# Kernel optimization log

Hardware: AMD Instinct MI355X
Metric: run time of the kernel (lower is better)

## Reference

```python
import jax, jax.numpy as jnp
import numpy as np

B, T, H, NC = 64, 512, 1000, 2000
WV, PV, IV, TV, MV = 100000, 50, 5, 20, 500
FEAT = 300 + 4 * 50  # 500
EPS = 1e-5


def setup_inputs() -> dict:
    key = jax.random.key(0)
    ks = jax.random.split(key, 32)

    def emb(k, v, d):
        t = jax.random.normal(k, (v, d), jnp.float32) * 0.1
        return t.at[0].set(0.0)  # padding_idx=0

    def unif(k, shape, s):
        return jax.random.uniform(k, shape, jnp.float32, -s, s)

    s = 1.0 / np.sqrt(H)
    inp = {}
    inp['word_idxs'] = jax.random.randint(ks[0], (B, T), 0, WV)
    inp['pos_idxs'] = jax.random.randint(ks[1], (B, T), 0, PV)
    inp['iob_idxs'] = jax.random.randint(ks[2], (B, T), 0, IV)
    inp['type_idxs'] = jax.random.randint(ks[3], (B, T), 0, TV)
    inp['mention_idxs'] = jax.random.randint(ks[4], (B, T), 0, MV)
    lengths = jnp.sort(jax.random.randint(ks[5], (B,), 1, T + 1))[::-1]
    inp['lengths'] = lengths.at[0].set(T)  # descending, max == T
    inp['hidden'] = jnp.zeros((2, B, H), jnp.float32)
    inp['word_emb'] = emb(ks[6], WV, 300)
    inp['pos_emb'] = emb(ks[7], PV, 50)
    inp['iob_emb'] = emb(ks[8], IV, 50)
    inp['type_emb'] = emb(ks[9], TV, 50)
    inp['mention_emb'] = emb(ks[10], MV, 50)
    inp['w_ih_fwd'] = unif(ks[11], (3 * H, FEAT), s)
    inp['w_hh_fwd'] = unif(ks[12], (3 * H, H), s)
    inp['b_ih_fwd'] = unif(ks[13], (3 * H,), s)
    inp['b_hh_fwd'] = unif(ks[14], (3 * H,), s)
    inp['w_ih_bwd'] = unif(ks[15], (3 * H, FEAT), s)
    inp['w_hh_bwd'] = unif(ks[16], (3 * H, H), s)
    inp['b_ih_bwd'] = unif(ks[17], (3 * H,), s)
    inp['b_hh_bwd'] = unif(ks[18], (3 * H,), s)
    inp['lin_w'] = unif(ks[19], (NC, 2 * H), 1.0 / np.sqrt(2 * H))
    inp['lin_b'] = unif(ks[20], (NC,), 1.0 / np.sqrt(2 * H))
    inp['bn_gamma'] = 1.0 + 0.1 * jax.random.normal(ks[21], (NC,), jnp.float32)
    inp['bn_beta'] = 0.1 * jax.random.normal(ks[22], (NC,), jnp.float32)
    inp['bn_mean'] = 0.1 * jax.random.normal(ks[23], (NC,), jnp.float32)
    inp['bn_var'] = jax.random.uniform(ks[24], (NC,), jnp.float32, 0.5, 1.5)
    return inp


def _gru_dir(x_proj, mask, h0, w_hh, b_hh):
    """x_proj: [T,B,3H] precomputed input projections; mask: [T,B] validity."""
    def step(h, tm):
        xp, m = tm
        hp = h @ w_hh.T + b_hh  # [B,3H]
        xr, xz, xn = jnp.split(xp, 3, axis=-1)
        hr, hz, hn = jnp.split(hp, 3, axis=-1)
        r = jax.nn.sigmoid(xr + hr)
        z = jax.nn.sigmoid(xz + hz)
        n = jnp.tanh(xn + r * hn)
        h_new = (1.0 - z) * n + z * h
        h = jnp.where(m[:, None], h_new, h)  # freeze past sequence end (packed semantics)
        return h, None
    hT, _ = jax.lax.scan(step, h0, (x_proj, mask))
    return hT


def reference(word_idxs, pos_idxs, iob_idxs, type_idxs, mention_idxs, lengths, hidden,
              word_emb, pos_emb, iob_emb, type_emb, mention_emb,
              w_ih_fwd, w_hh_fwd, b_ih_fwd, b_hh_fwd,
              w_ih_bwd, w_hh_bwd, b_ih_bwd, b_hh_bwd,
              lin_w, lin_b, bn_gamma, bn_beta, bn_mean, bn_var):
    # multi-embedding concat -> [B,T,500]; eval mode: dropouts identity
    feat = jnp.concatenate([
        word_emb[word_idxs], pos_emb[pos_idxs], iob_emb[iob_idxs],
        type_emb[type_idxs], mention_emb[mention_idxs]], axis=-1)
    valid = (jnp.arange(T)[None, :] < lengths[:, None])  # [B,T]

    # forward direction
    xpf = jnp.einsum('btf,gf->tbg', feat, w_ih_fwd) + b_ih_fwd  # [T,B,3H]
    h_f = _gru_dir(xpf, valid.T, hidden[0], w_hh_fwd, b_hh_fwd)

    # backward direction: reverse the valid portion of each sequence
    rev_idx = jnp.clip(lengths[:, None] - 1 - jnp.arange(T)[None, :], 0, T - 1)  # [B,T]
    feat_r = jnp.take_along_axis(feat, rev_idx[:, :, None], axis=1)
    xpb = jnp.einsum('btf,gf->tbg', feat_r, w_ih_bwd) + b_ih_bwd
    h_b = _gru_dir(xpb, valid.T, hidden[1], w_hh_bwd, b_hh_bwd)

    h_cat = jnp.concatenate([h_f, h_b], axis=-1)  # [B,2H]
    logits = h_cat @ lin_w.T + lin_b
    out = bn_gamma * (logits - bn_mean) * jax.lax.rsqrt(bn_var + EPS) + bn_beta
    hidden_out = jnp.stack([h_f, h_b])  # [2,B,H] like PyTorch GRU final hidden
    return out, hidden_out
```

## Files before the change

### kernel.cpp

```cpp
#include <hip/hip_runtime.h>
#include <hip/hip_bf16.h>

typedef __attribute__((ext_vector_type(8))) short bf16x8;
typedef __attribute__((ext_vector_type(4))) float f32x4;

#define MFMA16(a,b,c) __builtin_amdgcn_mfma_f32_16x16x32_bf16((a),(b),(c),0,0,0)

__device__ __forceinline__ float sigmf(float x){ return 1.f/(1.f + __expf(-x)); }
__device__ __forceinline__ float tanh_fast(float x){
    float e = __expf(-2.f*fabsf(x));
    float t = (1.f-e)/(1.f+e);
    return x < 0.f ? -t : t;
}

#define AS1 __attribute__((address_space(1)))
#define AS3 __attribute__((address_space(3)))
__device__ __forceinline__ void gll16(const void* g, void* l) {
    __builtin_amdgcn_global_load_lds((const AS1 unsigned int*)g, (AS3 unsigned int*)l, 16, 0, 0);
}

__device__ __forceinline__ bf16x8 load16_asm(const __hip_bfloat16* p) {
    bf16x8 v;
    asm volatile("global_load_dwordx4 %0, %1, off" : "=v"(v) : "v"(p));
    return v;
}
__device__ __forceinline__ bf16x8 load16_sc(const __hip_bfloat16* p) {
    bf16x8 v;
    asm volatile("global_load_dwordx4 %0, %1, off sc0 sc1" : "=v"(v) : "v"(p) : "memory");
    return v;
}
__device__ __forceinline__ void store2_sc(__hip_bfloat16* p, float v) {
    __hip_bfloat16 b = __float2bfloat16(v);
    unsigned int u = *reinterpret_cast<unsigned short*>(&b);
    asm volatile("global_store_short %0, %1, off sc0 sc1" :: "v"(p), "v"(u) : "memory");
}
__device__ __forceinline__ void store4_sc(unsigned* p, unsigned v) {
    asm volatile("global_store_dword %0, %1, off sc0 sc1" :: "v"(p), "v"(v) : "memory");
}
__device__ __forceinline__ unsigned poll_sc(const unsigned* p) {
    unsigned v;
    asm volatile("global_load_dword %0, %1, off sc0 sc1\n\ts_waitcnt vmcnt(0)"
                 : "=v"(v) : "v"(p) : "memory");
    return v;
}
__device__ __forceinline__ unsigned ld2_g(const __hip_bfloat16* p) {
    unsigned v;
    asm volatile("global_load_ushort %0, %1, off" : "=v"(v) : "v"(p));
    return v;
}

#define B_   64
#define T_   512
#define H_   1000
#define HP   1024
#define G3   3072
#define NC_  2000
#define FEAT_C 500
#define FEAT_P 512
#define NROWS 32768

#define OFF_FEAT  ((size_t)0)
#define OFF_WIHF  (OFF_FEAT + 33554432ull)
#define OFF_WIHB  (OFF_WIHF + 3145728ull)
#define OFF_WHH   (OFF_WIHB + 3145728ull)
#define OFF_LINW  (OFF_WHH + 12582912ull)
#define OFF_BIHF  (OFF_LINW + 8192000ull)
#define OFF_BIHB  (OFF_BIHF + 12288ull)
#define OFF_BHH   (OFF_BIHB + 12288ull)
#define OFF_XP    (OFF_BHH + 24576ull)
#define OFF_HBF   (OFF_XP + 402653184ull)
#define OFF_HCAT  (OFF_HBF + 524288ull)
#define OFF_BAR   (OFF_HCAT + 262144ull)
#define WS_NEED   (OFF_BAR + 1024ull)

__global__ void cvt_pad_3h(const float* __restrict__ src, __hip_bfloat16* __restrict__ dst,
                           int C, int Cp) {
    size_t i = (size_t)blockIdx.x*blockDim.x + threadIdx.x;
    size_t total = (size_t)G3 * Cp;
    if (i >= total) return;
    int r = (int)(i / Cp), c = (int)(i % Cp);
    int chunk = r >> 10, j = r & 1023;
    float v = (j < H_ && c < C) ? src[((size_t)chunk*H_ + j)*C + c] : 0.f;
    dst[i] = __float2bfloat16(v);
}

__global__ void cvt_pad(const float* __restrict__ src, __hip_bfloat16* __restrict__ dst,
                        int R, int C, int Cp) {
    size_t i = (size_t)blockIdx.x*blockDim.x + threadIdx.x;
    size_t total = (size_t)R * Cp;
    if (i >= total) return;
    int r = (int)(i / Cp), c = (int)(i % Cp);
    float v = (c < C) ? src[(size_t)r*C + c] : 0.f;
    dst[i] = __float2bfloat16(v);
}

__global__ void pad_b3h(const float* __restrict__ src, float* __restrict__ dst) {
    int i = blockIdx.x*blockDim.x + threadIdx.x;
    if (i >= G3) return;
    int chunk = i >> 10, j = i & 1023;
    dst[i] = (j < H_) ? src[chunk*H_ + j] : 0.f;
}

__global__ __launch_bounds__(256)
void embed_k(const int* __restrict__ wi, const int* __restrict__ pi, const int* __restrict__ ii,
             const int* __restrict__ ti, const int* __restrict__ mi,
             const float* __restrict__ we, const float* __restrict__ pe, const float* __restrict__ ie,
             const float* __restrict__ te, const float* __restrict__ me,
             __hip_bfloat16* __restrict__ feat) {
    int r = blockIdx.x;
    int iw = wi[r], ip = pi[r], ib = ii[r], it = ti[r], im = mi[r];
    #pragma unroll
    for (int q = 0; q < 2; ++q) {
        int c = threadIdx.x + q*256;
        float v;
        if      (c < 300) v = we[(size_t)iw*300 + c];
        else if (c < 350) v = pe[ip*50 + (c-300)];
        else if (c < 400) v = ie[ib*50 + (c-350)];
        else if (c < 450) v = te[it*50 + (c-400)];
        else if (c < 500) v = me[im*50 + (c-450)];
        else              v = 0.f;
        feat[(size_t)r*FEAT_P + c] = __float2bfloat16(v);
    }
}

__global__ __launch_bounds__(256)
void gemm_xp(const __hip_bfloat16* __restrict__ feat,
             const __hip_bfloat16* __restrict__ W,
             const float* __restrict__ bias,
             const int* __restrict__ lengths,
             __hip_bfloat16* __restrict__ xp,
             int dir) {
    __shared__ char smem_raw[32768];
    __hip_bfloat16* As = (__hip_bfloat16*)smem_raw;
    __hip_bfloat16* Bs = (__hip_bfloat16*)(smem_raw + 16384);
    const int tid = threadIdx.x;
    const int wave = tid >> 6, lane = tid & 63;
    const int bm = blockIdx.x, bn = blockIdx.y;
    const int wm = wave >> 1, wn = wave & 1;

    int arow_src[4];
    #pragma unroll
    for (int q = 0; q < 4; ++q) {
        int flat = q*256 + tid;
        int row = flat >> 3;
        int r_g = bm*128 + row;
        int t = r_g >> 6, b = r_g & 63;
        int src_t;
        if (dir == 0) src_t = t;
        else { int L = lengths[b]; src_t = L - 1 - t; src_t = src_t < 0 ? 0 : src_t; }
        arow_src[q] = b*T_ + src_t;
    }

    f32x4 acc[4][4];
    #pragma unroll
    for (int i = 0; i < 4; ++i)
        #pragma unroll
        for (int j = 0; j < 4; ++j) acc[i][j] = (f32x4){0.f,0.f,0.f,0.f};

    for (int kt = 0; kt < 8; ++kt) {
        int k0 = kt*64;
        #pragma unroll
        for (int q = 0; q < 4; ++q) {
            int flat = q*256 + tid;
            int row = flat >> 3, c8 = flat & 7;
            gll16(feat + (size_t)arow_src[q]*FEAT_P + k0 + c8*8,
                  As + (q*256 + wave*64)*8);
            gll16(W + (size_t)(bn*128 + row)*FEAT_P + k0 + c8*8,
                  Bs + (q*256 + wave*64)*8);
        }
        __syncthreads();
        #pragma unroll
        for (int ks = 0; ks < 2; ++ks) {
            bf16x8 af[4], bfr[4];
            #pragma unroll
            for (int i = 0; i < 4; ++i)
                af[i] = *(const bf16x8*)(As + (wm*64 + i*16 + (lane&15))*64 + ks*32 + (lane>>4)*8);
            #pragma unroll
            for (int j = 0; j < 4; ++j)
                bfr[j] = *(const bf16x8*)(Bs + (wn*64 + j*16 + (lane&15))*64 + ks*32 + (lane>>4)*8);
            #pragma unroll
            for (int i = 0; i < 4; ++i)
                #pragma unroll
                for (int j = 0; j < 4; ++j)
                    acc[i][j] = MFMA16(af[i], bfr[j], acc[i][j]);
        }
        __syncthreads();
    }

    __hip_bfloat16* Cs = (__hip_bfloat16*)smem_raw;
    #pragma unroll
    for (int j = 0; j < 4; ++j) {
        int col_l = wn*64 + j*16 + (lane & 15);
        float bs = bias[bn*128 + col_l];
        #pragma unroll
        for (int i = 0; i < 4; ++i) {
            #pragma unroll
            for (int r = 0; r < 4; ++r) {
                int row_l = wm*64 + i*16 + (lane>>4)*4 + r;
                Cs[row_l*128 + col_l] = __float2bfloat16(acc[i][j][r] + bs);
            }
        }
    }
    __syncthreads();
    #pragma unroll
    for (int q = 0; q < 8; ++q) {
        int flat = q*256 + tid;
        int row = flat >> 4, c8 = flat & 15;
        bf16x8 v = *(const bf16x8*)(Cs + row*128 + c8*8);
        *(bf16x8*)(xp + (size_t)(bm*128 + row)*G3 + bn*128 + c8*8) = v;
    }
}

__global__ void init_h(const float* __restrict__ hidden, __hip_bfloat16* __restrict__ hbf) {
    int i = blockIdx.x*blockDim.x + threadIdx.x;
    if (i >= 2*B_*HP) return;
    int row = i >> 10, j = i & 1023;
    int dir = row >> 6, b = row & 63;
    float v = (j < H_) ? hidden[((size_t)dir*B_ + b)*H_ + j] : 0.f;
    __hip_bfloat16 bv = __float2bfloat16(v);
    hbf[i] = bv;
    hbf[2*B_*HP + i] = bv;
}

__global__ void bar_init(unsigned* bar) { if (threadIdx.x < 256) bar[threadIdx.x] = 0u; }

__global__ __attribute__((amdgpu_flat_work_group_size(512,512), amdgpu_waves_per_eu(2,2)))
void gru_persist(const __hip_bfloat16* __restrict__ whh,
                 const float* __restrict__ bhh,
                 const __hip_bfloat16* __restrict__ xp,
                 const int* __restrict__ lengths,
                 const float* __restrict__ hidden,
                 __hip_bfloat16* __restrict__ hbf,
                 __hip_bfloat16* __restrict__ hcat,
                 float* __restrict__ hid_o,
                 unsigned* __restrict__ bar) {
    __shared__ float part[2][4][3][256];
    const int blk = blockIdx.x;
    const int r8  = blk & 7, q8 = blk >> 3;
    const int g   = r8 >> 1;
    const int dir = g >> 1, bh = g & 1;
    const int ug  = q8*2 + (r8 & 1);
    const int w    = threadIdx.x >> 6;
    const int lane = threadIdx.x & 63;
    const int bg  = w >> 2;
    const int kh  = w & 3;
    const int u   = lane & 15;
    const int rg  = lane >> 4;

    const int j   = ug*16 + u;
    const int bA  = bh*32 + bg*16 + u;
    const int bF  = bh*32 + bg*16 + rg*4 + kh;
    const int myLen  = lengths[bF];
    const int lenBlk = lengths[bh*32];

    unsigned* slots = bar + g*64;

    const float bhr = bhh[dir*G3 + j];
    const float bhz = bhh[dir*G3 + HP + j];
    const float bhn = bhh[dir*G3 + 2*HP + j];
    float hreg = (j < H_) ? hidden[((size_t)dir*B_ + bF)*H_ + j] : 0.f;

    bf16x8 wf0[8], wf1[8], wf2[8];
    {
        const __hip_bfloat16* wb = whh + (size_t)dir*G3*HP + (size_t)j*HP + kh*256 + rg*8;
        #pragma unroll
        for (int ks = 0; ks < 8; ++ks) {
            wf0[ks] = load16_asm(wb + ks*32);
            wf1[ks] = load16_asm(wb + (size_t)HP*HP + ks*32);
            wf2[ks] = load16_asm(wb + (size_t)2*HP*HP + ks*32);
        }
        asm volatile("s_waitcnt vmcnt(0)" ::: "memory");
        __builtin_amdgcn_sched_barrier(0);
    }

    const size_t hrowA = (size_t)(dir*B_ + bA)*HP + kh*256 + rg*8;
    const size_t hidxF = (size_t)(dir*B_ + bF)*HP + j;
    const size_t xbase = (size_t)dir*NROWS*G3 + (size_t)bF*G3 + j;

    unsigned pxr, pxz, pxn;
    {
        const __hip_bfloat16* x0 = xp + xbase;
        pxr = ld2_g(x0); pxz = ld2_g(x0 + HP); pxn = ld2_g(x0 + 2*HP);
        asm volatile("s_waitcnt vmcnt(0)" ::: "memory");
    }

    for (int t = 0; t < lenBlk; ++t) {
        const int cur = t & 1, prev = cur ^ 1;
        const __hip_bfloat16* ha = hbf + (size_t)prev*2*B_*HP + hrowA;
        bf16x8 af[8];
        #pragma unroll
        for (int ks = 0; ks < 8; ++ks) af[ks] = load16_sc(ha + ks*32);
        asm volatile("s_waitcnt vmcnt(0)" ::: "memory");
        __builtin_amdgcn_sched_barrier(0);

        f32x4 a0 = {0.f,0.f,0.f,0.f}, a1 = {0.f,0.f,0.f,0.f}, a2 = {0.f,0.f,0.f,0.f};
        #pragma unroll
        for (int ks = 0; ks < 8; ++ks) {
            a0 = MFMA16(af[ks], wf0[ks], a0);
            a1 = MFMA16(af[ks], wf1[ks], a1);
            a2 = MFMA16(af[ks], wf2[ks], a2);
        }

        float xr = __uint_as_float(pxr << 16);
        float xz = __uint_as_float(pxz << 16);
        float xn = __uint_as_float(pxn << 16);

        {
            int tn = (t + 1 < lenBlk) ? t + 1 : t;
            const __hip_bfloat16* xnp = xp + xbase + (size_t)tn*B_*G3;
            pxr = ld2_g(xnp); pxz = ld2_g(xnp + HP); pxn = ld2_g(xnp + 2*HP);
        }

        *(f32x4*)&part[bg][kh][0][lane*4] = a0;
        *(f32x4*)&part[bg][kh][1][lane*4] = a1;
        *(f32x4*)&part[bg][kh][2][lane*4] = a2;
        __syncthreads();
        float sr = 0.f, sz = 0.f, sn = 0.f;
        #pragma unroll
        for (int q = 0; q < 4; ++q) {
            sr += part[bg][q][0][lane*4 + kh];
            sz += part[bg][q][1][lane*4 + kh];
            sn += part[bg][q][2][lane*4 + kh];
        }
        float rr = sigmf(xr + sr + bhr);
        float zz = sigmf(xz + sz + bhz);
        float nn = tanh_fast(xn + rr*(sn + bhn));
        float hnew = (t < myLen) ? ((1.f - zz)*nn + zz*hreg) : hreg;
        hreg = hnew;
        store2_sc(hbf + (size_t)cur*2*B_*HP + hidxF, hnew);
        asm volatile("s_waitcnt vmcnt(0)" ::: "memory");
        __syncthreads();

        if (t + 1 < lenBlk) {
            if (w == 0) {
                if (lane == 0) store4_sc(&slots[ug], (unsigned)(t + 1));
                const unsigned tgt = (unsigned)(t + 1);
                for (;;) {
                    unsigned v = poll_sc(slots + lane);
                    if (__all((int)(v >= tgt))) break;
                    __builtin_amdgcn_s_sleep(1);
                }
            }
            __syncthreads();
        }
    }

    if (j < H_) {
        hid_o[((size_t)dir*B_ + bF)*H_ + j] = hreg;
        hcat[(size_t)bF*2048 + dir*H_ + j] = __float2bfloat16(hreg);
    }
}

__global__ __launch_bounds__(256)
void lin_bn_k(const __hip_bfloat16* __restrict__ hcat,
              const __hip_bfloat16* __restrict__ linw,
              const float* __restrict__ lin_b, const float* __restrict__ gamma,
              const float* __restrict__ beta, const float* __restrict__ mean,
              const float* __restrict__ var,
              float* __restrict__ out) {
    __shared__ __hip_bfloat16 wlds[16*2056];
    const int n0 = blockIdx.x*16;
    const int tid = threadIdx.x;
    #pragma unroll
    for (int q = 0; q < 16; ++q) {
        int flat8 = q*256 + tid;
        int row = flat8 >> 8, c8 = flat8 & 255;
        bf16x8 v = *(const bf16x8*)(linw + (size_t)(n0+row)*2048 + c8*8);
        *(bf16x8*)(wlds + row*2056 + c8*8) = v;
    }
    __syncthreads();
    const int wave = tid >> 6, lane = tid & 63;
    const int mrow = wave*16 + (lane & 15);
    f32x4 acc = {0.f,0.f,0.f,0.f};
    for (int ks = 0; ks < 64; ++ks) {
        bf16x8 a = *(const bf16x8*)(hcat + (size_t)mrow*2048 + ks*32 + (lane>>4)*8);
        bf16x8 b = *(const bf16x8*)(wlds + (lane&15)*2056 + ks*32 + (lane>>4)*8);
        acc = MFMA16(a, b, acc);
    }
    const int c = n0 + (lane & 15);
    const float g = gamma[c], bt = beta[c], mn = mean[c], lb = lin_b[c];
    const float iv = rsqrtf(var[c] + 1e-5f);
    #pragma unroll
    for (int r = 0; r < 4; ++r) {
        int b_ = wave*16 + (lane>>4)*4 + r;
        float logit = acc[r] + lb;
        out[(size_t)b_*NC_ + c] = g*(logit - mn)*iv + bt;
    }
}

extern "C" void kernel_launch(void* const* d_in, const int* in_sizes, int n_in,
                              void* d_out, int out_size, void* d_ws, size_t ws_size,
                              hipStream_t stream) {
    const int*   wi      = (const int*)d_in[0];
    const int*   pi      = (const int*)d_in[1];
    const int*   ii      = (const int*)d_in[2];
    const int*   ti      = (const int*)d_in[3];
    const int*   mi      = (const int*)d_in[4];
    const int*   lengths = (const int*)d_in[5];
    const float* hidden  = (const float*)d_in[6];
    const float* we      = (const float*)d_in[7];
    const float* pe      = (const float*)d_in[8];
    const float* ie      = (const float*)d_in[9];
    const float* te      = (const float*)d_in[10];
    const float* me      = (const float*)d_in[11];
    const float* w_ih_f  = (const float*)d_in[12];
    const float* w_hh_f  = (const float*)d_in[13];
    const float* b_ih_f  = (const float*)d_in[14];
    const float* b_hh_f  = (const float*)d_in[15];
    const float* w_ih_b  = (const float*)d_in[16];
    const float* w_hh_b  = (const float*)d_in[17];
    const float* b_ih_b  = (const float*)d_in[18];
    const float* b_hh_b  = (const float*)d_in[19];
    const float* lin_w   = (const float*)d_in[20];
    const float* lin_b   = (const float*)d_in[21];
    const float* gamma   = (const float*)d_in[22];
    const float* beta    = (const float*)d_in[23];
    const float* mean    = (const float*)d_in[24];
    const float* var     = (const float*)d_in[25];
    float* out = (float*)d_out;

    if (ws_size < WS_NEED) return;

    char* ws = (char*)d_ws;
    __hip_bfloat16* FEAT = (__hip_bfloat16*)(ws + OFF_FEAT);
    __hip_bfloat16* WIHF = (__hip_bfloat16*)(ws + OFF_WIHF);
    __hip_bfloat16* WIHB = (__hip_bfloat16*)(ws + OFF_WIHB);
    __hip_bfloat16* WHH  = (__hip_bfloat16*)(ws + OFF_WHH);
    __hip_bfloat16* LINW = (__hip_bfloat16*)(ws + OFF_LINW);
    float* BIHF = (float*)(ws + OFF_BIHF);
    float* BIHB = (float*)(ws + OFF_BIHB);
    float* BHH  = (float*)(ws + OFF_BHH);
    __hip_bfloat16* XP   = (__hip_bfloat16*)(ws + OFF_XP);
    __hip_bfloat16* HBF  = (__hip_bfloat16*)(ws + OFF_HBF);
    __hip_bfloat16* HCAT = (__hip_bfloat16*)(ws + OFF_HCAT);
    unsigned* BAR = (unsigned*)(ws + OFF_BAR);
    float* HIDO = out + (size_t)B_*NC_;

    cvt_pad_3h<<<(G3*512 + 255)/256, 256, 0, stream>>>(w_ih_f, WIHF, FEAT_C, FEAT_P);
    cvt_pad_3h<<<(G3*512 + 255)/256, 256, 0, stream>>>(w_ih_b, WIHB, FEAT_C, FEAT_P);
    cvt_pad_3h<<<(G3*1024 + 255)/256, 256, 0, stream>>>(w_hh_f, WHH, H_, HP);
    cvt_pad_3h<<<(G3*1024 + 255)/256, 256, 0, stream>>>(w_hh_b, WHH + (size_t)G3*HP, H_, HP);
    cvt_pad<<<(NC_*2048 + 255)/256, 256, 0, stream>>>(lin_w, LINW, NC_, NC_, 2048);
    pad_b3h<<<(G3 + 255)/256, 256, 0, stream>>>(b_ih_f, BIHF);
    pad_b3h<<<(G3 + 255)/256, 256, 0, stream>>>(b_ih_b, BIHB);
    pad_b3h<<<(G3 + 255)/256, 256, 0, stream>>>(b_hh_f, BHH);
    pad_b3h<<<(G3 + 255)/256, 256, 0, stream>>>(b_hh_b, BHH + G3);

    embed_k<<<NROWS, 256, 0, stream>>>(wi, pi, ii, ti, mi, we, pe, ie, te, me, FEAT);

    dim3 gg(NROWS/128, G3/128);
    gemm_xp<<<gg, 256, 0, stream>>>(FEAT, WIHF, BIHF, lengths, XP, 0);
    gemm_xp<<<gg, 256, 0, stream>>>(FEAT, WIHB, BIHB, lengths, XP + (size_t)NROWS*G3, 1);

    init_h<<<(2*B_*HP + 255)/256, 256, 0, stream>>>(hidden, HBF);
    bar_init<<<1, 256, 0, stream>>>(BAR);
    {
        void* args[] = { (void*)&WHH, (void*)&BHH, (void*)&XP, (void*)&lengths,
                         (void*)&hidden, (void*)&HBF, (void*)&HCAT, (void*)&HIDO, (void*)&BAR };
        hipLaunchCooperativeKernel((const void*)gru_persist, dim3(256), dim3(512),
                                   args, 0, stream);
    }

    lin_bn_k<<<NC_/16, 256, 0, stream>>>(HCAT, LINW, lin_b, gamma, beta, mean, var, out);
}
```

Measured before the change: 3.490 ms.

## Repartition persistent GRU across 128 blocks with LDS-staged hidden state

Reworks the persistent GRU kernel from 256 blocks in groups of 64 over 32 batches to 128 blocks in groups of 16 over 16 batches per direction. Each block now loads its 16-row hidden slice into LDS once and shares it across waves, keeps twice as many W_hh fragments in registers per wave, and uses a two-way K split instead of a four-way one. Input projections are fetched as 16-byte vector loads staged through LDS rather than per-thread scalar loads. Barrier slots are spaced onto separate cache lines and each group waits on only 16 peers. In exchange, half as many CUs run the step, there is more register pressure, and there is an extra LDS round-trip and __syncthreads per step.

```diff
diff --git a/kernel.cpp b/kernel.cpp
--- a/kernel.cpp
+++ b/kernel.cpp
@@ -43,11 +43,9 @@
                  : "=v"(v) : "v"(p) : "memory");
     return v;
 }
-__device__ __forceinline__ unsigned ld2_g(const __hip_bfloat16* p) {
-    unsigned v;
-    asm volatile("global_load_ushort %0, %1, off" : "=v"(v) : "v"(p));
-    return v;
-}
+
+#define VDRAIN() do { asm volatile("s_waitcnt vmcnt(0)" ::: "memory"); \
+                      __builtin_amdgcn_sched_barrier(0); } while (0)
 
 #define B_   64
 #define T_   512
@@ -58,6 +56,11 @@
 #define FEAT_C 500
 #define FEAT_P 512
 #define NROWS 32768
+
+#define HROW 2064
+#define OFF_PART  (16*HROW)
+#define OFF_XPLDS (OFF_PART + 12288)
+#define SMEM_SZ   (OFF_XPLDS + 6144)
 
 #define OFF_FEAT  ((size_t)0)
 #define OFF_WIHF  (OFF_FEAT + 33554432ull)
@@ -71,7 +74,7 @@
 #define OFF_HBF   (OFF_XP + 402653184ull)
 #define OFF_HCAT  (OFF_HBF + 524288ull)
 #define OFF_BAR   (OFF_HCAT + 262144ull)
-#define WS_NEED   (OFF_BAR + 1024ull)
+#define WS_NEED   (OFF_BAR + 8192ull)
 
 __global__ void cvt_pad_3h(const float* __restrict__ src, __hip_bfloat16* __restrict__ dst,
                            int C, int Cp) {
@@ -222,7 +225,10 @@
     hbf[2*B_*HP + i] = bv;
 }
 
-__global__ void bar_init(unsigned* bar) { if (threadIdx.x < 256) bar[threadIdx.x] = 0u; }
+__global__ void bar_init(unsigned* bar) {
+    int i = blockIdx.x*blockDim.x + threadIdx.x;
+    if (i < 2048) bar[i] = 0u;
+}
 
 __global__ __attribute__((amdgpu_flat_work_group_size(512,512), amdgpu_waves_per_eu(2,2)))
 void gru_persist(const __hip_bfloat16* __restrict__ whh,
@@ -234,109 +240,137 @@
                  __hip_bfloat16* __restrict__ hcat,
                  float* __restrict__ hid_o,
                  unsigned* __restrict__ bar) {
-    __shared__ float part[2][4][3][256];
+    __shared__ char smem[SMEM_SZ];
+    char*  hlds  = smem;
+    float* part  = (float*)(smem + OFF_PART);
+    __hip_bfloat16* xplds = (__hip_bfloat16*)(smem + OFF_XPLDS);
+
     const int blk = blockIdx.x;
-    const int r8  = blk & 7, q8 = blk >> 3;
-    const int g   = r8 >> 1;
-    const int dir = g >> 1, bh = g & 1;
-    const int ug  = q8*2 + (r8 & 1);
-    const int w    = threadIdx.x >> 6;
-    const int lane = threadIdx.x & 63;
-    const int bg  = w >> 2;
-    const int kh  = w & 3;
-    const int u   = lane & 15;
-    const int rg  = lane >> 4;
-
-    const int j   = ug*16 + u;
-    const int bA  = bh*32 + bg*16 + u;
-    const int bF  = bh*32 + bg*16 + rg*4 + kh;
-    const int myLen  = lengths[bF];
-    const int lenBlk = lengths[bh*32];
-
-    unsigned* slots = bar + g*64;
-
+    const int g   = blk >> 4;
+    const int ub  = blk & 15;
+    const int dir = g >> 2, bq = g & 3;
+    const int tid  = threadIdx.x;
+    const int w    = tid >> 6;
+    const int lane = tid & 63;
+    const int cg   = w >> 1;
+    const int kh2  = w & 1;
+    const int u    = lane & 15;
+    const int rg   = lane >> 4;
+
+    const int j = ub*64 + cg*16 + u;
+    const int lenBlk = lengths[bq*16];
+
+    unsigned* slots = bar + g*256;
+
+    float hreg[4]; int lenr[4];
+    #pragma unroll
+    for (int e = 0; e < 4; ++e) {
+        int b = bq*16 + rg*4 + e;
+        lenr[e] = lengths[b];
+        hreg[e] = (j < H_) ? hidden[((size_t)dir*B_ + b)*H_ + j] : 0.f;
+    }
     const float bhr = bhh[dir*G3 + j];
     const float bhz = bhh[dir*G3 + HP + j];
     const float bhn = bhh[dir*G3 + 2*HP + j];
-    float hreg = (j < H_) ? hidden[((size_t)dir*B_ + bF)*H_ + j] : 0.f;
-
-    bf16x8 wf0[8], wf1[8], wf2[8];
+
+    bf16x8 wr0[16], wr1[16], wr2[16];
     {
-        const __hip_bfloat16* wb = whh + (size_t)dir*G3*HP + (size_t)j*HP + kh*256 + rg*8;
+        const __hip_bfloat16* wb = whh + (size_t)dir*G3*HP + (size_t)j*HP + kh2*512 + rg*8;
         #pragma unroll
-        for (int ks = 0; ks < 8; ++ks) {
-            wf0[ks] = load16_asm(wb + ks*32);
-            wf1[ks] = load16_asm(wb + (size_t)HP*HP + ks*32);
-            wf2[ks] = load16_asm(wb + (size_t)2*HP*HP + ks*32);
-        }
-        asm volatile("s_waitcnt vmcnt(0)" ::: "memory");
-        __builtin_amdgcn_sched_barrier(0);
-    }
-
-    const size_t hrowA = (size_t)(dir*B_ + bA)*HP + kh*256 + rg*8;
-    const size_t hidxF = (size_t)(dir*B_ + bF)*HP + j;
-    const size_t xbase = (size_t)dir*NROWS*G3 + (size_t)bF*G3 + j;
-
-    unsigned pxr, pxz, pxn;
-    {
-        const __hip_bfloat16* x0 = xp + xbase;
-        pxr = ld2_g(x0); pxz = ld2_g(x0 + HP); pxn = ld2_g(x0 + 2*HP);
-        asm volatile("s_waitcnt vmcnt(0)" ::: "memory");
-    }
+        for (int ks = 0; ks < 16; ++ks) {
+            wr0[ks] = load16_asm(wb + ks*32);
+            wr1[ks] = load16_asm(wb + (size_t)HP*HP + ks*32);
+            wr2[ks] = load16_asm(wb + (size_t)2*HP*HP + ks*32);
+        }
+    }
+    VDRAIN();
+
+    const bool xthr = (tid < 384);
+    const int xgate = tid >> 7;
+    const int xr4   = (tid & 127) >> 3;
+    const int xc8   = tid & 7;
+    const __hip_bfloat16* xsrc0 = xp + (size_t)dir*NROWS*G3
+        + ((size_t)bq*16 + xr4)*G3 + (size_t)xgate*HP + ub*64 + xc8*8;
+    const int xoff = xgate*1024 + xr4*64 + xc8*8;
+
+    bf16x8 pxp = {};
+    if (xthr) pxp = load16_asm(xsrc0);
 
     for (int t = 0; t < lenBlk; ++t) {
         const int cur = t & 1, prev = cur ^ 1;
-        const __hip_bfloat16* ha = hbf + (size_t)prev*2*B_*HP + hrowA;
-        bf16x8 af[8];
-        #pragma unroll
-        for (int ks = 0; ks < 8; ++ks) af[ks] = load16_sc(ha + ks*32);
-        asm volatile("s_waitcnt vmcnt(0)" ::: "memory");
-        __builtin_amdgcn_sched_barrier(0);
+
+        {
+            const __hip_bfloat16* hb = hbf + (size_t)prev*2*B_*HP
+                                       + ((size_t)dir*B_ + bq*16)*HP;
+            bf16x8 hv[4];
+            #pragma unroll
+            for (int q = 0; q < 4; ++q) {
+                int flat = q*512 + tid;
+                int row = flat >> 7, c16 = flat & 127;
+                hv[q] = load16_sc(hb + row*HP + c16*8);
+            }
+            VDRAIN();
+            #pragma unroll
+            for (int q = 0; q < 4; ++q) {
+                int flat = q*512 + tid;
+                int row = flat >> 7, c16 = flat & 127;
+                *(bf16x8*)(hlds + row*HROW + c16*16) = hv[q];
+            }
+            if (xthr) *(bf16x8*)(xplds + xoff) = pxp;
+        }
+        __syncthreads();
 
         f32x4 a0 = {0.f,0.f,0.f,0.f}, a1 = {0.f,0.f,0.f,0.f}, a2 = {0.f,0.f,0.f,0.f};
-        #pragma unroll
-        for (int ks = 0; ks < 8; ++ks) {
-            a0 = MFMA16(af[ks], wf0[ks], a0);
-            a1 = MFMA16(af[ks], wf1[ks], a1);
-            a2 = MFMA16(af[ks], wf2[ks], a2);
-        }
-
-        float xr = __uint_as_float(pxr << 16);
-        float xz = __uint_as_float(pxz << 16);
-        float xn = __uint_as_float(pxn << 16);
-
         {
-            int tn = (t + 1 < lenBlk) ? t + 1 : t;
-            const __hip_bfloat16* xnp = xp + xbase + (size_t)tn*B_*G3;
-            pxr = ld2_g(xnp); pxz = ld2_g(xnp + HP); pxn = ld2_g(xnp + 2*HP);
-        }
-
-        *(f32x4*)&part[bg][kh][0][lane*4] = a0;
-        *(f32x4*)&part[bg][kh][1][lane*4] = a1;
-        *(f32x4*)&part[bg][kh][2][lane*4] = a2;
+            const int abase = u*HROW + kh2*1024 + rg*16;
+            #pragma unroll
+            for (int ks = 0; ks < 16; ++ks) {
+                bf16x8 a = *(const bf16x8*)(hlds + abase + ks*64);
+                a0 = MFMA16(a, wr0[ks], a0);
+                a1 = MFMA16(a, wr1[ks], a1);
+                a2 = MFMA16(a, wr2[ks], a2);
+            }
+        }
+
+        if (kh2 == 1) {
+            *(f32x4*)&part[((cg*3 + 0)*64 + lane)*4] = a0;
+            *(f32x4*)&part[((cg*3 + 1)*64 + lane)*4] = a1;
+            *(f32x4*)&part[((cg*3 + 2)*64 + lane)*4] = a2;
+        }
         __syncthreads();
-        float sr = 0.f, sz = 0.f, sn = 0.f;
-        #pragma unroll
-        for (int q = 0; q < 4; ++q) {
-            sr += part[bg][q][0][lane*4 + kh];
-            sz += part[bg][q][1][lane*4 + kh];
-            sn += part[bg][q][2][lane*4 + kh];
-        }
-        float rr = sigmf(xr + sr + bhr);
-        float zz = sigmf(xz + sz + bhz);
-        float nn = tanh_fast(xn + rr*(sn + bhn));
-        float hnew = (t < myLen) ? ((1.f - zz)*nn + zz*hreg) : hreg;
-        hreg = hnew;
-        store2_sc(hbf + (size_t)cur*2*B_*HP + hidxF, hnew);
-        asm volatile("s_waitcnt vmcnt(0)" ::: "memory");
+
+        if (kh2 == 0) {
+            f32x4 p0 = *(const f32x4*)&part[((cg*3 + 0)*64 + lane)*4];
+            f32x4 p1 = *(const f32x4*)&part[((cg*3 + 1)*64 + lane)*4];
+            f32x4 p2 = *(const f32x4*)&part[((cg*3 + 2)*64 + lane)*4];
+            a0 += p0; a1 += p1; a2 += p2;
+            __hip_bfloat16* hc = hbf + (size_t)cur*2*B_*HP
+                                 + ((size_t)dir*B_ + bq*16)*HP + j;
+            const int xcol = cg*16 + u;
+            #pragma unroll
+            for (int e = 0; e < 4; ++e) {
+                int row = rg*4 + e;
+                float xvr = __bfloat162float(xplds[0*1024 + row*64 + xcol]);
+                float xvz = __bfloat162float(xplds[1*1024 + row*64 + xcol]);
+                float xvn = __bfloat162float(xplds[2*1024 + row*64 + xcol]);
+                float rr = sigmf(xvr + a0[e] + bhr);
+                float zz = sigmf(xvz + a1[e] + bhz);
+                float nn = tanh_fast(xvn + rr*(a2[e] + bhn));
+                float hnew = (t < lenr[e]) ? ((1.f - zz)*nn + zz*hreg[e]) : hreg[e];
+                hreg[e] = hnew;
+                store2_sc(hc + row*HP, hnew);
+            }
+        }
+        VDRAIN();
         __syncthreads();
 
         if (t + 1 < lenBlk) {
+            if (xthr) pxp = load16_asm(xsrc0 + (size_t)(t+1)*B_*G3);
             if (w == 0) {
-                if (lane == 0) store4_sc(&slots[ug], (unsigned)(t + 1));
+                if (lane == 0) store4_sc(&slots[ub*16], (unsigned)(t + 1));
                 const unsigned tgt = (unsigned)(t + 1);
                 for (;;) {
-                    unsigned v = poll_sc(slots + lane);
+                    unsigned v = poll_sc(slots + (lane & 15)*16);
                     if (__all((int)(v >= tgt))) break;
                     __builtin_amdgcn_s_sleep(1);
                 }
@@ -345,9 +379,17 @@
         }
     }
 
-    if (j < H_) {
-        hid_o[((size_t)dir*B_ + bF)*H_ + j] = hreg;
-        hcat[(size_t)bF*2048 + dir*H_ + j] = __float2bfloat16(hreg);
+    if (kh2 == 0) {
+        #pragma unroll
+        for (int e = 0; e < 4; ++e) {
+            int b = bq*16 + rg*4 + e;
+            if (j < H_) {
+                hid_o[((size_t)dir*B_ + b)*H_ + j] = hreg[e];
+                hcat[(size_t)b*2048 + dir*H_ + j] = __float2bfloat16(hreg[e]);
+            } else {
+                hcat[(size_t)b*2048 + 2000 + dir*24 + (j - H_)] = __float2bfloat16(0.f);
+            }
+        }
     }
 }
 
@@ -453,11 +495,11 @@
     gemm_xp<<<gg, 256, 0, stream>>>(FEAT, WIHB, BIHB, lengths, XP + (size_t)NROWS*G3, 1);
 
     init_h<<<(2*B_*HP + 255)/256, 256, 0, stream>>>(hidden, HBF);
-    bar_init<<<1, 256, 0, stream>>>(BAR);
+    bar_init<<<8, 256, 0, stream>>>(BAR);
     {
         void* args[] = { (void*)&WHH, (void*)&BHH, (void*)&XP, (void*)&lengths,
                          (void*)&hidden, (void*)&HBF, (void*)&HCAT, (void*)&HIDO, (void*)&BAR };
-        hipLaunchCooperativeKernel((const void*)gru_persist, dim3(256), dim3(512),
+        hipLaunchCooperativeKernel((const void*)gru_persist, dim3(128), dim3(512),
                                    args, 0, stream);
     }
 
```

Result: slower. 3.656 ms (+4.8%).
